# Kernel optimization log

Hardware: AMD Instinct MI355X
Metric: run time of the kernel (lower is better)

Reference implementation:

```python
import jax, jax.numpy as jnp
from jax import lax
import numpy as np

B, T, H, L = 4096, 7, 512, 256
D = 2 * H  # bidirectional LSTM feature dim


def _lstm(x, wih, whh, bih, bhh, reverse):
    # x: [B, T, L]; torch gate order i, f, g, o
    b, hdim = x.shape[0], whh.shape[0]
    xs = jnp.swapaxes(x, 0, 1)  # [T, B, L]
    bias = bih + bhh

    def step(carry, xt):
        h, c = carry
        gates = xt @ wih + h @ whh + bias
        i, f, g, o = jnp.split(gates, 4, axis=-1)
        c = jax.nn.sigmoid(f) * c + jax.nn.sigmoid(i) * jnp.tanh(g)
        h = jax.nn.sigmoid(o) * jnp.tanh(c)
        return (h, c), h

    h0 = jnp.zeros((b, hdim), x.dtype)
    _, hs = lax.scan(step, (h0, h0), xs, reverse=reverse)
    return jnp.swapaxes(hs, 0, 1)  # [B, T, H]


def _att(enc, dec):
    # Sequential attention: keys/values start as enc and grow with each decoder output.
    keys = enc  # [B, T, D]
    outs = []
    for i in range(dec.shape[1]):  # fixed small T=7, Python loop is static
        q = dec[:, i, :]                                  # [B, D]
        scores = jnp.einsum('bd,btd->bt', q, keys)        # dot over features
        a = jax.nn.softmax(scores, axis=1)
        ctx = jnp.einsum('bt,btd->bd', a, keys)
        out = ctx + q
        outs.append(out)
        keys = jnp.concatenate([keys, out[:, None, :]], axis=1)
    return jnp.stack(outs, axis=1)  # [B, T, D]


def _deconv(x, w, b):
    # torch ConvTranspose2d (stride 1, pad 0) == full conv with flipped, in/out-swapped kernel
    kh, kw = w.shape[2], w.shape[3]
    w2 = jnp.transpose(w[:, :, ::-1, ::-1], (1, 0, 2, 3))  # [out, in, kh, kw]
    y = lax.conv_general_dilated(x, w2, (1, 1), ((kh - 1, kh - 1), (kw - 1, kw - 1)),
                                 dimension_numbers=('NCHW', 'OIHW', 'NCHW'))
    return y + b[None, :, None, None]


def setup_inputs() -> dict:
    key = jax.random.key(0)
    ks = jax.random.split(key, 12)
    p = lambda k, shape: jax.random.normal(k, shape, jnp.float32) * 0.02
    return {
        'lstm_enc': jax.random.normal(ks[0], (B, T, D), jnp.float32),
        'gaussian_noise': jax.random.normal(ks[1], (B, L), jnp.float32),
        'embedrep_w': p(ks[2], (L, L * T)), 'embedrep_b': jnp.zeros((L * T,), jnp.float32),
        'wih_f': p(ks[3], (L, 4 * H)), 'whh_f': p(ks[4], (H, 4 * H)),
        'bih_f': jnp.zeros((4 * H,), jnp.float32), 'bhh_f': jnp.zeros((4 * H,), jnp.float32),
        'wih_b': p(ks[5], (L, 4 * H)), 'whh_b': p(ks[6], (H, 4 * H)),
        'bih_b': jnp.zeros((4 * H,), jnp.float32), 'bhh_b': jnp.zeros((4 * H,), jnp.float32),
        'emb_w': p(ks[7], (D, 1024)), 'emb_b': jnp.zeros((1024,), jnp.float32),
        'dc3_w': p(ks[8], (64, 32, 1, 3)), 'dc3_b': jnp.zeros((32,), jnp.float32),
        'dc1_w': p(ks[9], (32, 16, 1, 5)), 'dc1_b': jnp.zeros((16,), jnp.float32),
        'dc2_w': p(ks[10], (16, 1, 3, 3)), 'dc2_b': jnp.zeros((1,), jnp.float32),
        'infer': 0,
    }


def reference(lstm_enc, gaussian_noise, embedrep_w, embedrep_b,
              wih_f, whh_f, bih_f, bhh_f, wih_b, whh_b, bih_b, bhh_b,
              emb_w, emb_b, dc3_w, dc3_b, dc1_w, dc1_b, dc2_w, dc2_b, infer):
    b = lstm_enc.shape[0]
    g1 = jax.nn.soft_sign(gaussian_noise @ embedrep_w + embedrep_b)   # [B, L*T]
    rep = g1.reshape(b, T, L)                                          # [B, 7, L]
    hf = _lstm(rep, wih_f, whh_f, bih_f, bhh_f, False)
    hb = _lstm(rep, wih_b, whh_b, bih_b, bhh_b, True)
    lstm1 = jnp.concatenate([hf, hb], axis=-1)                         # [B, 7, 2H]
    att_out = _att(lstm_enc, lstm1)                                    # [B, 7, 2H]
    emb = att_out @ emb_w + emb_b                                      # [B, 7, 1024]
    up = jax.nn.soft_sign(emb).reshape(b * T, 64, 1, 16)
    x = jax.nn.leaky_relu(_deconv(up, dc3_w, dc3_b))                   # [B*7, 32, 1, 18]
    x = jax.nn.leaky_relu(_deconv(x, dc1_w, dc1_b))                    # [B*7, 16, 1, 22]
    x = jax.nn.leaky_relu(_deconv(x, dc2_w, dc2_b))                    # [B*7, 1, 3, 24]
    x = jax.nn.softmax(x, axis=2)                                      # softmax over H dim (=3)
    out = x.reshape(b, T, 1, 3, 24)[:, :, -1, :, :]                    # [B, 7, 3, 24]
    return out
```

## Files before the change

### kernel.cpp

```cpp
#include <hip/hip_runtime.h>
#include <stdint.h>


typedef __attribute__((ext_vector_type(4))) float f32x4;
typedef __attribute__((ext_vector_type(8))) short bf16x8;
typedef __attribute__((ext_vector_type(4))) unsigned short us4;

__device__ __forceinline__ unsigned short f2b(float f) {
  union { float f; unsigned u; } x; x.f = f;
  unsigned r = x.u + 0x7FFFu + ((x.u >> 16) & 1u);
  return (unsigned short)(r >> 16);
}
__device__ __forceinline__ float b2f(unsigned short s) {
  union { unsigned u; float f; } x; x.u = ((unsigned)s) << 16; return x.f;
}
__device__ __forceinline__ float sigmoidf(float x) {
  return 1.f / (1.f + __expf(-x));
}
__device__ __forceinline__ float fast_tanh(float x) {
  x = fminf(15.f, fmaxf(-15.f, x));
  float e = __expf(2.f * x);
  return (e - 1.f) / (e + 1.f);
}

__device__ __forceinline__ void gl_lds16(const void* g, void* l) {
  auto gp = reinterpret_cast<const __attribute__((address_space(1))) unsigned int*>(
      reinterpret_cast<uintptr_t>(g));
  auto lp = reinterpret_cast<__attribute__((address_space(3))) unsigned int*>(
      reinterpret_cast<uintptr_t>(l));
  __builtin_amdgcn_global_load_lds(gp, lp, 16, 0, 0);
}

__device__ __forceinline__ void stage256x64_swz(const unsigned short* src, int ld,
                                                unsigned short* lds, int tid) {
  const int wv = tid >> 6;
  const int g = (tid & 7) ^ ((tid >> 3) & 7);
  const int rowin = tid >> 3;
#pragma unroll
  for (int r = 0; r < 4; ++r) {
    int row = r * 64 + rowin;
    gl_lds16(src + (size_t)row * ld + g * 8, lds + r * 4096 + wv * 512);
  }
}

__device__ __forceinline__ bf16x8 lds_frag(const unsigned short* base, int row, int ko) {
  return *(const bf16x8*)(base + row * 64 + (ko ^ ((row & 7) << 3)));
}

__device__ __forceinline__ void ktile_256(const unsigned short* As, const unsigned short* Bs,
                                          int wm, int wn, int lane, f32x4 acc[8][4]) {
  const int lr = lane & 15, lq = (lane >> 4) * 8;
  bf16x8 b[4][2];
#pragma unroll
  for (int ni = 0; ni < 4; ++ni) {
    int brow = wn * 64 + ni * 16 + lr;
    b[ni][0] = lds_frag(Bs, brow, lq);
    b[ni][1] = lds_frag(Bs, brow, 32 + lq);
  }
#pragma unroll
  for (int mi = 0; mi < 8; ++mi) {
    int arow = wm * 128 + mi * 16 + lr;
    bf16x8 a0 = lds_frag(As, arow, lq);
    bf16x8 a1 = lds_frag(As, arow, 32 + lq);
#pragma unroll
    for (int ni = 0; ni < 4; ++ni) {
      acc[mi][ni] = __builtin_amdgcn_mfma_f32_16x16x32_bf16(a0, b[ni][0], acc[mi][ni], 0, 0, 0);
      acc[mi][ni] = __builtin_amdgcn_mfma_f32_16x16x32_bf16(a1, b[ni][1], acc[mi][ni], 0, 0, 0);
    }
  }
}

#define KLOOP_GATE(kt, NT)                                         \
  if ((kt) + 1 < (NT)) asm volatile("s_waitcnt vmcnt(8)" ::: "memory"); \
  else                 asm volatile("s_waitcnt vmcnt(0)" ::: "memory"); \
  __builtin_amdgcn_s_barrier();                                    \
  __builtin_amdgcn_sched_barrier(0);

#define KLOOP_FREE()                                               \
  __builtin_amdgcn_sched_barrier(0);                               \
  __builtin_amdgcn_s_barrier();

__device__ __forceinline__ void stage128x64(const unsigned short* src, int ld,
                                            unsigned short* lds, int wv, int lane) {
#pragma unroll
  for (int r = 0; r < 4; ++r) {
    int row = r * 32 + wv * 8 + (lane >> 3);
    gl_lds16(src + (size_t)row * ld + (lane & 7) * 8, lds + (r * 32 + wv * 8) * 64);
  }
}
__device__ __forceinline__ void mfma_tile(const unsigned short* As, const unsigned short* Bs,
                                          int wm, int wn, int lane, f32x4 acc[4][4]) {
#pragma unroll
  for (int kk = 0; kk < 2; ++kk) {
    int ko = kk * 32 + (lane >> 4) * 8;
    bf16x8 a[4], b[4];
#pragma unroll
    for (int i = 0; i < 4; ++i)
      a[i] = *(const bf16x8*)(As + (size_t)(wm * 64 + i * 16 + (lane & 15)) * 64 + ko);
#pragma unroll
    for (int i = 0; i < 4; ++i)
      b[i] = *(const bf16x8*)(Bs + (size_t)(wn * 64 + i * 16 + (lane & 15)) * 64 + ko);
#pragma unroll
    for (int mi = 0; mi < 4; ++mi)
#pragma unroll
      for (int ni = 0; ni < 4; ++ni)
        acc[mi][ni] = __builtin_amdgcn_mfma_f32_16x16x32_bf16(a[mi], b[ni], acc[mi][ni], 0, 0, 0);
  }
}

__global__ __launch_bounds__(256) void pack_kernel(
    const float* __restrict__ noise, const float* __restrict__ erep_w,
    const float* __restrict__ emb_w,
    const float* __restrict__ wih_f, const float* __restrict__ whh_f,
    const float* __restrict__ bih_f, const float* __restrict__ bhh_f,
    const float* __restrict__ wih_b, const float* __restrict__ whh_b,
    const float* __restrict__ bih_b, const float* __restrict__ bhh_b,
    unsigned short* __restrict__ noiseb, unsigned short* __restrict__ erepT,
    unsigned short* __restrict__ embT, unsigned short* __restrict__ lstmW,
    float* __restrict__ lstmB) {
  const int N0 = 4096 * 256;
  const int N1 = 1792 * 256;
  const int N2 = 1024 * 1024;
  const int N3 = 2 * 2048 * 768;
  const int N4 = 2 * 2048;
  const int total = N0 + N1 + N2 + N3 + N4;
  for (int i = blockIdx.x * 256 + threadIdx.x; i < total; i += gridDim.x * 256) {
    int x = i;
    if (x < N0) { noiseb[x] = f2b(noise[x]); continue; }
    x -= N0;
    if (x < N1) { int n = x >> 8, k = x & 255; erepT[x] = f2b(erep_w[k * 1792 + n]); continue; }
    x -= N1;
    if (x < N2) {
      int n = x >> 10, k = x & 1023;
      int o = (n & 63) * 16 + (n >> 6);
      embT[x] = f2b(emb_w[k * 1024 + o]);
      continue;
    }
    x -= N2;
    if (x < N3) {
      int dir = x / (2048 * 768);
      int r = x - dir * (2048 * 768);
      int npk = r / 768, k = r - (r / 768) * 768;
      int blk = npk >> 6, g = (npk >> 4) & 3, u = npk & 15;
      int o = g * 512 + blk * 16 + u;
      const float* wih = dir ? wih_b : wih_f;
      const float* whh = dir ? whh_b : whh_f;
      float v = (k < 256) ? wih[k * 2048 + o] : whh[(k - 256) * 2048 + o];
      lstmW[x] = f2b(v);
      continue;
    }
    x -= N3;
    {
      int dir = x >> 11, npk = x & 2047;
      int blk = npk >> 6, g = (npk >> 4) & 3, u = npk & 15;
      int o = g * 512 + blk * 16 + u;
      lstmB[x] = dir ? (bih_b[o] + bhh_b[o]) : (bih_f[o] + bhh_f[o]);
    }
  }
}

__global__ __launch_bounds__(256) void gemm_rep_kernel(
    const unsigned short* __restrict__ A, const unsigned short* __restrict__ Bt,
    const float* __restrict__ bias, unsigned short* __restrict__ rep_t) {
  __shared__ unsigned short As[128 * 64];
  __shared__ unsigned short Bs[128 * 64];
  const int lane = threadIdx.x & 63, wv = threadIdx.x >> 6;
  const int wm = wv >> 1, wn = wv & 1;
  const int m0 = blockIdx.y * 128, n0 = blockIdx.x * 128;
  f32x4 acc[4][4];
#pragma unroll
  for (int i = 0; i < 4; ++i)
#pragma unroll
    for (int j = 0; j < 4; ++j) acc[i][j] = (f32x4){0.f, 0.f, 0.f, 0.f};
  for (int k0 = 0; k0 < 256; k0 += 64) {
    stage128x64(A + (size_t)m0 * 256 + k0, 256, As, wv, lane);
    stage128x64(Bt + (size_t)n0 * 256 + k0, 256, Bs, wv, lane);
    __syncthreads();
    mfma_tile(As, Bs, wm, wn, lane, acc);
    __syncthreads();
  }
#pragma unroll
  for (int ni = 0; ni < 4; ++ni) {
    int n = n0 + wn * 64 + ni * 16 + (lane & 15);
    float bv = bias[n];
    int t = n >> 8, l = n & 255;
#pragma unroll
    for (int mi = 0; mi < 4; ++mi)
#pragma unroll
      for (int r = 0; r < 4; ++r) {
        int m = m0 + wm * 64 + mi * 16 + (lane >> 4) * 4 + r;
        float v = acc[mi][ni][r] + bv;
        v = v / (1.f + fabsf(v));
        rep_t[((size_t)t * 4096 + m) * 256 + l] = f2b(v);
      }
  }
}

__global__ __launch_bounds__(512, 2) void lstm_step256_kernel(
    const unsigned short* __restrict__ rep_t, const unsigned short* __restrict__ Wp,
    const float* __restrict__ biasP, unsigned short* __restrict__ hbuf,
    float* __restrict__ cbuf, unsigned short* __restrict__ lstm1, int step) {
  __shared__ unsigned short AsB[2][256 * 64];
  __shared__ unsigned short BsB[2][256 * 64];
  const int tid = threadIdx.x, lane = tid & 63, wv = tid >> 6;
  const int wm = wv >> 2, wn = wv & 3;
  const int swz = (blockIdx.x & 7) * 32 + (blockIdx.x >> 3);
  const int dir = swz >> 7;
  const int by = (swz & 127) >> 3, bx = swz & 7;
  const int m0 = by * 256, n0 = bx * 256;
  const int t_proc = dir ? (6 - step) : step;
  const unsigned short* W = Wp + (size_t)dir * 2048 * 768;
  const unsigned short* hin = hbuf + ((size_t)(step & 1) * 2 + dir) * (4096 * 512);
  unsigned short* hout = hbuf + ((size_t)((step + 1) & 1) * 2 + dir) * (4096 * 512);
  float* cp = cbuf + (size_t)dir * (4096 * 512);
  const unsigned short* xsrc = rep_t + (size_t)t_proc * 4096 * 256;

  f32x4 acc[8][4];
#pragma unroll
  for (int i = 0; i < 8; ++i)
#pragma unroll
    for (int j = 0; j < 4; ++j) acc[i][j] = (f32x4){0.f, 0.f, 0.f, 0.f};

#define LSTM_STAGE_A(kt, buf)                                                     \
  if ((kt) < 4) stage256x64_swz(xsrc + (size_t)m0 * 256 + (kt) * 64, 256, AsB[buf], tid); \
  else          stage256x64_swz(hin + (size_t)m0 * 512 + ((kt) - 4) * 64, 512, AsB[buf], tid);

  LSTM_STAGE_A(0, 0)
  stage256x64_swz(W + (size_t)n0 * 768 + 0, 768, BsB[0], tid);
  LSTM_STAGE_A(1, 1)
  stage256x64_swz(W + (size_t)n0 * 768 + 64, 768, BsB[1], tid);

  for (int kt = 0; kt < 12; ++kt) {
    const int cur = kt & 1;
    KLOOP_GATE(kt, 12)
    ktile_256(AsB[cur], BsB[cur], wm, wn, lane, acc);
    KLOOP_FREE()
    if (kt + 2 < 12) {
      LSTM_STAGE_A(kt + 2, cur)
      stage256x64_swz(W + (size_t)n0 * 768 + (kt + 2) * 64, 768, BsB[cur], tid);
    }
  }
#undef LSTM_STAGE_A

  const int u = lane & 15;
  const int blk = (n0 + wn * 64) >> 6;
  const int j = blk * 16 + u;
  const float bz0 = biasP[dir * 2048 + blk * 64 + 0 * 16 + u];
  const float bz1 = biasP[dir * 2048 + blk * 64 + 1 * 16 + u];
  const float bz2 = biasP[dir * 2048 + blk * 64 + 2 * 16 + u];
  const float bz3 = biasP[dir * 2048 + blk * 64 + 3 * 16 + u];
#pragma unroll
  for (int mi = 0; mi < 8; ++mi)
#pragma unroll
    for (int r = 0; r < 4; ++r) {
      int row = m0 + wm * 128 + mi * 16 + (lane >> 4) * 4 + r;
      float gi = acc[mi][0][r] + bz0;
      float gf = acc[mi][1][r] + bz1;
      float gg = acc[mi][2][r] + bz2;
      float go = acc[mi][3][r] + bz3;
      size_t ci = (size_t)row * 512 + j;
      float c = sigmoidf(gf) * cp[ci] + sigmoidf(gi) * fast_tanh(gg);
      cp[ci] = c;
      float h = sigmoidf(go) * fast_tanh(c);
      unsigned short hb = f2b(h);
      hout[ci] = hb;
      lstm1[((size_t)row * 7 + t_proc) * 1024 + dir * 512 + j] = hb;
    }
}

__global__ __launch_bounds__(256) void att_fused2_kernel(
    const float* __restrict__ enc, const unsigned short* __restrict__ lstm1,
    unsigned short* __restrict__ att) {
  __shared__ unsigned short Qs[7 * 1032];
  __shared__ unsigned short Ehs[7 * 1032];
  __shared__ unsigned short Els[7 * 1032];
  __shared__ float P[4 * 2 * 64 * 4];
  __shared__ float sG[98];
  __shared__ float sC[7][14];
  __shared__ float sA[16];
  const int tid = threadIdx.x, lane = tid & 63, wv = tid >> 6;
  const int b = blockIdx.x;
  const float* Eb = enc + (size_t)b * 7168;
  const unsigned short* Qb = lstm1 + (size_t)b * 7168;

  if (tid < 98) ((float*)sC)[tid] = 0.f;

  const f32x4* Eb4 = (const f32x4*)Eb;
#pragma unroll
  for (int r = 0; r < 7; ++r) {
    f32x4 v = Eb4[r * 256 + tid];
    us4 hi, lo;
#pragma unroll
    for (int e = 0; e < 4; ++e) {
      hi[e] = f2b(v[e]);
      lo[e] = f2b(v[e] - b2f(hi[e]));
    }
    *(us4*)&Ehs[r * 1032 + tid * 4] = hi;
    *(us4*)&Els[r * 1032 + tid * 4] = lo;
  }
  const bf16x8* Qb8 = (const bf16x8*)Qb;
#pragma unroll
  for (int r = 0; r < 4; ++r) {
    int idx = r * 256 + tid;
    if (idx < 896) {
      int row = idx >> 7, col = (idx & 127) * 8;
      *(bf16x8*)&Qs[row * 1032 + col] = Qb8[idx];
    }
  }
  __syncthreads();

  {
    const int rr = lane & 15;
    const int rowc = rr > 6 ? 6 : rr;
    const int kbase = wv * 256 + (lane >> 4) * 8;
    f32x4 g1 = {0.f, 0.f, 0.f, 0.f}, g2 = {0.f, 0.f, 0.f, 0.f};
#pragma unroll
    for (int s = 0; s < 8; ++s) {
      const int k0 = kbase + s * 32;
      bf16x8 aq = *(const bf16x8*)&Qs[rowc * 1032 + k0];
      bf16x8 bh = *(const bf16x8*)&Ehs[rowc * 1032 + k0];
      bf16x8 bl = *(const bf16x8*)&Els[rowc * 1032 + k0];
      g1 = __builtin_amdgcn_mfma_f32_16x16x32_bf16(aq, bh, g1, 0, 0, 0);
      g1 = __builtin_amdgcn_mfma_f32_16x16x32_bf16(aq, bl, g1, 0, 0, 0);
      g2 = __builtin_amdgcn_mfma_f32_16x16x32_bf16(aq, aq, g2, 0, 0, 0);
    }
    *(f32x4*)&P[((wv * 2 + 0) * 64 + lane) * 4] = g1;
    *(f32x4*)&P[((wv * 2 + 1) * 64 + lane) * 4] = g2;
  }
  __syncthreads();

  if (tid < 98) {
    int i = tid / 14, v = tid - i * 14;
    int col = v < 7 ? v : v - 7;
    int tile = v < 7 ? 0 : 1;
    int ln = ((i >> 2) << 4) | col;
    int rg = i & 3;
    float s = 0.f;
#pragma unroll
    for (int w = 0; w < 4; ++w) s += P[((w * 2 + tile) * 64 + ln) * 4 + rg];
    sG[i * 14 + v] = s;
  }
  __syncthreads();

  if (wv == 0) {
    for (int i = 0; i < 7; ++i) {
      const int nt = 7 + i;
      float s = -1e30f;
      if (lane < 7) {
        s = sG[i * 14 + lane];
      } else if (lane < nt) {
        int jj = lane - 7;
        float a2 = 0.f;
#pragma unroll
        for (int v = 0; v < 14; ++v) a2 += sC[jj][v] * sG[i * 14 + v];
        s = a2;
      }
      float mx = s;
#pragma unroll
      for (int off = 8; off >= 1; off >>= 1) mx = fmaxf(mx, __shfl_xor(mx, off, 16));
      float e = (lane < nt) ? __expf(s - mx) : 0.f;
      float sum = e;
#pragma unroll
      for (int off = 8; off >= 1; off >>= 1) sum += __shfl_xor(sum, off, 16);
      float a = e / sum;
      if (lane < 16) sA[lane] = a;
      if (lane < 14) {
        float c = (lane < 7) ? sA[lane] : 0.f;
        for (int jj = 0; jj < i; ++jj) c += sA[7 + jj] * sC[jj][lane];
        if (lane == 7 + i) c += 1.f;
        sC[i][lane] = c;
      }
    }
  }
  __syncthreads();

  {
    const int d0 = tid * 4;
    float acc[7][4];
#pragma unroll
    for (int i = 0; i < 7; ++i)
#pragma unroll
      for (int e = 0; e < 4; ++e) acc[i][e] = 0.f;
#pragma unroll
    for (int t = 0; t < 7; ++t) {
      us4 h = *(const us4*)&Ehs[t * 1032 + d0];
      us4 l = *(const us4*)&Els[t * 1032 + d0];
      float ev[4];
#pragma unroll
      for (int e = 0; e < 4; ++e) ev[e] = b2f(h[e]) + b2f(l[e]);
#pragma unroll
      for (int i = 0; i < 7; ++i) {
        float c = sC[i][t];
#pragma unroll
        for (int e = 0; e < 4; ++e) acc[i][e] += c * ev[e];
      }
    }
#pragma unroll
    for (int m = 0; m < 7; ++m) {
      us4 qv = *(const us4*)&Qs[m * 1032 + d0];
      float qf[4];
#pragma unroll
      for (int e = 0; e < 4; ++e) qf[e] = b2f(qv[e]);
#pragma unroll
      for (int i = m; i < 7; ++i) {
        float c = sC[i][7 + m];
#pragma unroll
        for (int e = 0; e < 4; ++e) acc[i][e] += c * qf[e];
      }
    }
    unsigned short* Ab = att + (size_t)b * 7168;
#pragma unroll
    for (int i = 0; i < 7; ++i) {
      us4 r;
#pragma unroll
      for (int e = 0; e < 4; ++e) r[e] = f2b(acc[i][e]);
      *(us4*)(Ab + i * 1024 + d0) = r;
    }
  }
}

__global__ __launch_bounds__(512, 2) void gemm_emb256_kernel(
    const unsigned short* __restrict__ A, const unsigned short* __restrict__ Bt,
    const float* __restrict__ bias, unsigned short* __restrict__ up_t) {
  __shared__ unsigned short AsB[2][256 * 64];
  __shared__ unsigned short BsB[2][256 * 64];
  const int tid = threadIdx.x, lane = tid & 63, wv = tid >> 6;
  const int wm = wv >> 2, wn = wv & 3;
  const int swz = (blockIdx.x & 7) * 56 + (blockIdx.x >> 3);
  const int by = swz >> 2, bx = swz & 3;
  const int m0 = by * 256, n0 = bx * 256;

  f32x4 acc[8][4];
#pragma unroll
  for (int i = 0; i < 8; ++i)
#pragma unroll
    for (int j = 0; j < 4; ++j) acc[i][j] = (f32x4){0.f, 0.f, 0.f, 0.f};

  stage256x64_swz(A + (size_t)m0 * 1024 + 0, 1024, AsB[0], tid);
  stage256x64_swz(Bt + (size_t)n0 * 1024 + 0, 1024, BsB[0], tid);
  stage256x64_swz(A + (size_t)m0 * 1024 + 64, 1024, AsB[1], tid);
  stage256x64_swz(Bt + (size_t)n0 * 1024 + 64, 1024, BsB[1], tid);

  for (int kt = 0; kt < 16; ++kt) {
    const int cur = kt & 1;
    KLOOP_GATE(kt, 16)
    ktile_256(AsB[cur], BsB[cur], wm, wn, lane, acc);
    KLOOP_FREE()
    if (kt + 2 < 16) {
      stage256x64_swz(A + (size_t)m0 * 1024 + (kt + 2) * 64, 1024, AsB[cur], tid);
      stage256x64_swz(Bt + (size_t)n0 * 1024 + (kt + 2) * 64, 1024, BsB[cur], tid);
    }
  }

#pragma unroll
  for (int ni = 0; ni < 4; ++ni) {
    int np = n0 + wn * 64 + ni * 16 + (lane & 15);
    int o = (np & 63) * 16 + (np >> 6);
    float bv = bias[o];
#pragma unroll
    for (int mi = 0; mi < 8; ++mi)
#pragma unroll
      for (int r = 0; r < 4; ++r) {
        int m = m0 + wm * 128 + mi * 16 + (lane >> 4) * 4 + r;
        float v = acc[mi][ni][r] + bv;
        v = v / (1.f + fabsf(v));
        up_t[(size_t)m * 1024 + np] = f2b(v);
      }
  }
}

__global__ __launch_bounds__(256) void dc3_kernel(const unsigned short* __restrict__ up_t,
                                                  const float* __restrict__ w3,
                                                  const float* __restrict__ b3,
                                                  unsigned short* __restrict__ y1_t) {
  const int lane = threadIdx.x & 63, wv = threadIdx.x >> 6;
  const int kq = (lane >> 4) * 8;
  const int oc = lane & 15;
  bf16x8 bf[2][6];
#pragma unroll
  for (int nt = 0; nt < 2; ++nt)
#pragma unroll
    for (int kk = 0; kk < 6; ++kk) {
      bf16x8 v;
#pragma unroll
      for (int t = 0; t < 8; ++t) {
        int k = kk * 32 + kq + t;
        int jj = k >> 6, ic = k & 63;
        v[t] = (short)f2b(w3[((size_t)ic * 32 + nt * 16 + oc) * 3 + jj]);
      }
      bf[nt][kk] = v;
    }
  const float bia0 = b3[oc], bia1 = b3[16 + oc];
  const int base_chunk = blockIdx.x * 32 + wv * 8;
  for (int cc = 0; cc < 8; ++cc) {
    const int chunk = base_chunk + cc;
    int m = chunk * 16 + (lane & 15);
    int img = m / 18, ow = m - img * 18;
    const unsigned short* arow = up_t + (size_t)img * 1024;
    f32x4 acc0 = {0.f, 0.f, 0.f, 0.f}, acc1 = {0.f, 0.f, 0.f, 0.f};
#pragma unroll
    for (int kk = 0; kk < 6; ++kk) {
      int jj = kk >> 1;
      int ic0 = (kk & 1) * 32 + kq;
      int iw = ow - jj;
      bf16x8 a = {0, 0, 0, 0, 0, 0, 0, 0};
      if ((unsigned)iw < 16u) a = *(const bf16x8*)(arow + iw * 64 + ic0);
      acc0 = __builtin_amdgcn_mfma_f32_16x16x32_bf16(a, bf[0][kk], acc0, 0, 0, 0);
      acc1 = __builtin_amdgcn_mfma_f32_16x16x32_bf16(a, bf[1][kk], acc1, 0, 0, 0);
    }
#pragma unroll
    for (int r = 0; r < 4; ++r) {
      int mm = chunk * 16 + (lane >> 4) * 4 + r;
      float v0 = acc0[r] + bia0; v0 = v0 > 0.f ? v0 : 0.01f * v0;
      float v1 = acc1[r] + bia1; v1 = v1 > 0.f ? v1 : 0.01f * v1;
      y1_t[(size_t)mm * 32 + oc] = f2b(v0);
      y1_t[(size_t)mm * 32 + 16 + oc] = f2b(v1);
    }
  }
}

__global__ __launch_bounds__(256) void dc1_kernel(const unsigned short* __restrict__ y1_t,
                                                  const float* __restrict__ w1,
                                                  const float* __restrict__ b1,
                                                  unsigned short* __restrict__ y2_t) {
  const int lane = threadIdx.x & 63, wv = threadIdx.x >> 6;
  const int kq = (lane >> 4) * 8;
  const int oc = lane & 15;
  bf16x8 bf[5];
#pragma unroll
  for (int kk = 0; kk < 5; ++kk) {
    bf16x8 v;
#pragma unroll
    for (int t = 0; t < 8; ++t) {
      int ic = kq + t;
      v[t] = (short)f2b(w1[((size_t)ic * 16 + oc) * 5 + kk]);
    }
    bf[kk] = v;
  }
  const float bia = b1[oc];
  const int base_chunk = blockIdx.x * 32 + wv * 8;
  for (int cc = 0; cc < 8; ++cc) {
    const int chunk = base_chunk + cc;
    int m = chunk * 16 + (lane & 15);
    int img = m / 22, ow = m - img * 22;
    const unsigned short* abase = y1_t + (size_t)img * 18 * 32;
    f32x4 acc = {0.f, 0.f, 0.f, 0.f};
#pragma unroll
    for (int kk = 0; kk < 5; ++kk) {
      int iw = ow - kk;
      bf16x8 a = {0, 0, 0, 0, 0, 0, 0, 0};
      if ((unsigned)iw < 18u) a = *(const bf16x8*)(abase + iw * 32 + kq);
      acc = __builtin_amdgcn_mfma_f32_16x16x32_bf16(a, bf[kk], acc, 0, 0, 0);
    }
#pragma unroll
    for (int r = 0; r < 4; ++r) {
      int mm = chunk * 16 + (lane >> 4) * 4 + r;
      float v = acc[r] + bia;
      v = v > 0.f ? v : 0.01f * v;
      y2_t[(size_t)mm * 16 + oc] = f2b(v);
    }
  }
}

__global__ __launch_bounds__(256) void dc2_kernel(const unsigned short* __restrict__ y2_t,
                                                  const float* __restrict__ w2,
                                                  const float* __restrict__ b2,
                                                  float* __restrict__ out) {
  int idx = blockIdx.x * 256 + threadIdx.x;
  int img = idx / 24, ow = idx - img * 24;
  float lg0 = b2[0], lg1 = b2[0], lg2 = b2[0];
#pragma unroll
  for (int jj = 0; jj < 3; ++jj) {
    int iw = ow - jj;
    if ((unsigned)iw >= 22u) continue;
    const unsigned short* row = y2_t + ((size_t)img * 22 + iw) * 16;
    bf16x8 v0 = *(const bf16x8*)(row);
    bf16x8 v1 = *(const bf16x8*)(row + 8);
    float x[16];
#pragma unroll
    for (int ic = 0; ic < 8; ++ic) {
      x[ic] = b2f((unsigned short)v0[ic]);
      x[8 + ic] = b2f((unsigned short)v1[ic]);
    }
#pragma unroll
    for (int ic = 0; ic < 16; ++ic) {
      lg0 += x[ic] * w2[ic * 9 + 0 * 3 + jj];
      lg1 += x[ic] * w2[ic * 9 + 1 * 3 + jj];
      lg2 += x[ic] * w2[ic * 9 + 2 * 3 + jj];
    }
  }
  lg0 = lg0 > 0.f ? lg0 : 0.01f * lg0;
  lg1 = lg1 > 0.f ? lg1 : 0.01f * lg1;
  lg2 = lg2 > 0.f ? lg2 : 0.01f * lg2;
  float mx = fmaxf(lg0, fmaxf(lg1, lg2));
  float e0 = __expf(lg0 - mx), e1 = __expf(lg1 - mx), e2 = __expf(lg2 - mx);
  float inv = 1.f / (e0 + e1 + e2);
  size_t ob = (size_t)img * 72 + ow;
  out[ob] = e0 * inv;
  out[ob + 24] = e1 * inv;
  out[ob + 48] = e2 * inv;
}

extern "C" void kernel_launch(void* const* d_in, const int* in_sizes, int n_in,
                              void* d_out, int out_size, void* d_ws, size_t ws_size,
                              hipStream_t stream) {
  (void)in_sizes; (void)n_in; (void)out_size; (void)ws_size;
  const float* enc    = (const float*)d_in[0];
  const float* noise  = (const float*)d_in[1];
  const float* erep_w = (const float*)d_in[2];
  const float* erep_b = (const float*)d_in[3];
  const float* wih_f  = (const float*)d_in[4];
  const float* whh_f  = (const float*)d_in[5];
  const float* bih_f  = (const float*)d_in[6];
  const float* bhh_f  = (const float*)d_in[7];
  const float* wih_b  = (const float*)d_in[8];
  const float* whh_b  = (const float*)d_in[9];
  const float* bih_b  = (const float*)d_in[10];
  const float* bhh_b  = (const float*)d_in[11];
  const float* emb_w  = (const float*)d_in[12];
  const float* emb_b  = (const float*)d_in[13];
  const float* dc3w   = (const float*)d_in[14];
  const float* dc3b   = (const float*)d_in[15];
  const float* dc1w   = (const float*)d_in[16];
  const float* dc1b   = (const float*)d_in[17];
  const float* dc2w   = (const float*)d_in[18];
  const float* dc2b   = (const float*)d_in[19];
  float* out = (float*)d_out;

  char* p = (char*)d_ws;
  auto carve = [&p](size_t bytes) {
    char* r = p;
    p += (bytes + 255) & ~(size_t)255;
    return r;
  };
  unsigned short* rep_t  = (unsigned short*)carve(7ull * 4096 * 256 * 2);
  unsigned short* lstmW  = (unsigned short*)carve(2ull * 2048 * 768 * 2);
  float*          lstmB  = (float*)carve(2ull * 2048 * 4);
  unsigned short* noiseb = (unsigned short*)carve(4096ull * 256 * 2);
  unsigned short* erepT  = (unsigned short*)carve(1792ull * 256 * 2);
  unsigned short* embT   = (unsigned short*)carve(1024ull * 1024 * 2);
  unsigned short* hbuf   = (unsigned short*)carve(4ull * 4096 * 512 * 2);
  float*          cbuf   = (float*)carve(2ull * 4096 * 512 * 4);
  unsigned short* lstm1  = (unsigned short*)carve(4096ull * 7 * 1024 * 2);
  unsigned short* att    = (unsigned short*)carve(28672ull * 1024 * 2);
  unsigned short* up_t   = (unsigned short*)carve(28672ull * 1024 * 2);
  unsigned short* y1_t   = (unsigned short*)carve(28672ull * 18 * 32 * 2);
  unsigned short* y2_t   = (unsigned short*)carve(28672ull * 22 * 16 * 2);

  hipMemsetAsync(hbuf, 0, 2ull * 4096 * 512 * 2, stream);
  hipMemsetAsync(cbuf, 0, 2ull * 4096 * 512 * 4, stream);

  pack_kernel<<<2048, 256, 0, stream>>>(noise, erep_w, emb_w, wih_f, whh_f, bih_f, bhh_f,
                                        wih_b, whh_b, bih_b, bhh_b,
                                        noiseb, erepT, embT, lstmW, lstmB);
  gemm_rep_kernel<<<dim3(14, 32), 256, 0, stream>>>(noiseb, erepT, erep_b, rep_t);
  for (int s = 0; s < 7; ++s)
    lstm_step256_kernel<<<256, 512, 0, stream>>>(rep_t, lstmW, lstmB, hbuf, cbuf, lstm1, s);
  att_fused2_kernel<<<4096, 256, 0, stream>>>(enc, lstm1, att);
  gemm_emb256_kernel<<<448, 512, 0, stream>>>(att, embT, emb_b, up_t);
  dc3_kernel<<<1008, 256, 0, stream>>>(up_t, dc3w, dc3b, y1_t);
  dc1_kernel<<<1232, 256, 0, stream>>>(y1_t, dc1w, dc1b, y2_t);
  dc2_kernel<<<2688, 256, 0, stream>>>(y2_t, dc2w, dc2b, out);
}
```

Before: 533.0 us.

## Split K-tiles into half-tiles with fine-grained 8-phase staged MFMA pipeline

Replaces the double-buffered 256x64 K-tile loop in the LSTM step and embedding GEMM kernels with a pipeline over 32-wide half-tiles. Each half-tile is computed in two MFMA phases, and global-to-LDS loads for later half-tiles are issued between phases, gated by per-phase vmcnt waits and barriers. It also adds setprio around the MFMA bursts and a new LDS swizzle for 32-element rows. The aim is to overlap memory traffic with compute more finely and cut pipeline bubbles, at the cost of more barriers and tighter, more fragile waitcnt accounting.

```diff
diff --git a/kernel.cpp b/kernel.cpp
--- a/kernel.cpp
+++ b/kernel.cpp
@@ -31,54 +31,55 @@
   __builtin_amdgcn_global_load_lds(gp, lp, 16, 0, 0);
 }
 
-__device__ __forceinline__ void stage256x64_swz(const unsigned short* src, int ld,
-                                                unsigned short* lds, int tid) {
-  const int wv = tid >> 6;
-  const int g = (tid & 7) ^ ((tid >> 3) & 7);
-  const int rowin = tid >> 3;
-#pragma unroll
-  for (int r = 0; r < 4; ++r) {
-    int row = r * 64 + rowin;
-    gl_lds16(src + (size_t)row * ld + g * 8, lds + r * 4096 + wv * 512);
-  }
-}
-
-__device__ __forceinline__ bf16x8 lds_frag(const unsigned short* base, int row, int ko) {
-  return *(const bf16x8*)(base + row * 64 + (ko ^ ((row & 7) << 3)));
-}
-
-__device__ __forceinline__ void ktile_256(const unsigned short* As, const unsigned short* Bs,
-                                          int wm, int wn, int lane, f32x4 acc[8][4]) {
+
+__device__ __forceinline__ void stage_half(const unsigned short* src, int ld,
+                                           unsigned short* hbase, int tid) {
+  const int row_in = tid >> 2;
+  const int gidx = tid & 3;
+#pragma unroll
+  for (int r = 0; r < 2; ++r) {
+    int row = r * 128 + row_in;
+    int gsrc = gidx ^ ((row >> 1) & 3);
+    gl_lds16(src + (size_t)row * ld + gsrc * 8, hbase + r * 4096 + (tid >> 6) * 512);
+  }
+}
+
+__device__ __forceinline__ bf16x8 lds_fragH(const unsigned short* hbase, int row, int lq) {
+  return *(const bf16x8*)(hbase + row * 32 + (lq ^ (((row >> 1) & 3) << 3)));
+}
+
+__device__ __forceinline__ void gate8() { asm volatile("s_waitcnt vmcnt(8)" ::: "memory"); }
+__device__ __forceinline__ void gate4() { asm volatile("s_waitcnt vmcnt(4)" ::: "memory"); }
+__device__ __forceinline__ void gate0() { asm volatile("s_waitcnt vmcnt(0)" ::: "memory"); }
+
+#define PH_TOP()                         \
+  __builtin_amdgcn_s_barrier();          \
+  __builtin_amdgcn_sched_barrier(0)
+
+template<int MH, bool READB>
+__device__ __forceinline__ void phase_mfma(const unsigned short* Ah, const unsigned short* Bh,
+                                           int wm, int wn, int lane,
+                                           bf16x8 (&bfr)[4], f32x4 (&acc)[8][4]) {
   const int lr = lane & 15, lq = (lane >> 4) * 8;
-  bf16x8 b[4][2];
-#pragma unroll
-  for (int ni = 0; ni < 4; ++ni) {
-    int brow = wn * 64 + ni * 16 + lr;
-    b[ni][0] = lds_frag(Bs, brow, lq);
-    b[ni][1] = lds_frag(Bs, brow, 32 + lq);
-  }
-#pragma unroll
-  for (int mi = 0; mi < 8; ++mi) {
-    int arow = wm * 128 + mi * 16 + lr;
-    bf16x8 a0 = lds_frag(As, arow, lq);
-    bf16x8 a1 = lds_frag(As, arow, 32 + lq);
-#pragma unroll
-    for (int ni = 0; ni < 4; ++ni) {
-      acc[mi][ni] = __builtin_amdgcn_mfma_f32_16x16x32_bf16(a0, b[ni][0], acc[mi][ni], 0, 0, 0);
-      acc[mi][ni] = __builtin_amdgcn_mfma_f32_16x16x32_bf16(a1, b[ni][1], acc[mi][ni], 0, 0, 0);
-    }
-  }
-}
-
-#define KLOOP_GATE(kt, NT)                                         \
-  if ((kt) + 1 < (NT)) asm volatile("s_waitcnt vmcnt(8)" ::: "memory"); \
-  else                 asm volatile("s_waitcnt vmcnt(0)" ::: "memory"); \
-  __builtin_amdgcn_s_barrier();                                    \
+  if (READB) {
+#pragma unroll
+    for (int ni = 0; ni < 4; ++ni) bfr[ni] = lds_fragH(Bh, wn * 64 + ni * 16 + lr, lq);
+  }
+  bf16x8 a[4];
+#pragma unroll
+  for (int i = 0; i < 4; ++i)
+    a[i] = lds_fragH(Ah, wm * 128 + (MH * 4 + i) * 16 + lr, lq);
+  asm volatile("s_waitcnt lgkmcnt(0)" ::: "memory");
   __builtin_amdgcn_sched_barrier(0);
-
-#define KLOOP_FREE()                                               \
-  __builtin_amdgcn_sched_barrier(0);                               \
-  __builtin_amdgcn_s_barrier();
+  __builtin_amdgcn_s_setprio(1);
+#pragma unroll
+  for (int i = 0; i < 4; ++i)
+#pragma unroll
+    for (int ni = 0; ni < 4; ++ni)
+      acc[MH * 4 + i][ni] =
+          __builtin_amdgcn_mfma_f32_16x16x32_bf16(a[i], bfr[ni], acc[MH * 4 + i][ni], 0, 0, 0);
+  __builtin_amdgcn_s_setprio(0);
+}
 
 __device__ __forceinline__ void stage128x64(const unsigned short* src, int ld,
                                             unsigned short* lds, int wv, int lane) {
@@ -200,8 +201,8 @@
     const unsigned short* __restrict__ rep_t, const unsigned short* __restrict__ Wp,
     const float* __restrict__ biasP, unsigned short* __restrict__ hbuf,
     float* __restrict__ cbuf, unsigned short* __restrict__ lstm1, int step) {
-  __shared__ unsigned short AsB[2][256 * 64];
-  __shared__ unsigned short BsB[2][256 * 64];
+  __shared__ unsigned short Ax[2][2][8192];
+  __shared__ unsigned short Bx[2][2][8192];
   const int tid = threadIdx.x, lane = tid & 63, wv = tid >> 6;
   const int wm = wv >> 2, wn = wv & 3;
   const int swz = (blockIdx.x & 7) * 32 + (blockIdx.x >> 3);
@@ -221,26 +222,53 @@
 #pragma unroll
     for (int j = 0; j < 4; ++j) acc[i][j] = (f32x4){0.f, 0.f, 0.f, 0.f};
 
-#define LSTM_STAGE_A(kt, buf)                                                     \
-  if ((kt) < 4) stage256x64_swz(xsrc + (size_t)m0 * 256 + (kt) * 64, 256, AsB[buf], tid); \
-  else          stage256x64_swz(hin + (size_t)m0 * 512 + ((kt) - 4) * 64, 512, AsB[buf], tid);
-
-  LSTM_STAGE_A(0, 0)
-  stage256x64_swz(W + (size_t)n0 * 768 + 0, 768, BsB[0], tid);
-  LSTM_STAGE_A(1, 1)
-  stage256x64_swz(W + (size_t)n0 * 768 + 64, 768, BsB[1], tid);
-
-  for (int kt = 0; kt < 12; ++kt) {
-    const int cur = kt & 1;
-    KLOOP_GATE(kt, 12)
-    ktile_256(AsB[cur], BsB[cur], wm, wn, lane, acc);
-    KLOOP_FREE()
-    if (kt + 2 < 12) {
-      LSTM_STAGE_A(kt + 2, cur)
-      stage256x64_swz(W + (size_t)n0 * 768 + (kt + 2) * 64, 768, BsB[cur], tid);
-    }
-  }
-#undef LSTM_STAGE_A
+#define ASRC_L(kt, h) ((kt) < 4 ? xsrc + (size_t)m0 * 256 + (kt) * 64 + (h) * 32 \
+                                : hin + (size_t)m0 * 512 + ((kt) - 4) * 64 + (h) * 32)
+#define ALD_L(kt) ((kt) < 4 ? 256 : 512)
+#define BSRC_L(kt, h) (W + (size_t)n0 * 768 + (kt) * 64 + (h) * 32)
+
+  stage_half(ASRC_L(0, 0), ALD_L(0), Ax[0][0], tid);
+  stage_half(BSRC_L(0, 0), 768, Bx[0][0], tid);
+  stage_half(ASRC_L(0, 1), ALD_L(0), Ax[0][1], tid);
+  stage_half(BSRC_L(0, 1), 768, Bx[0][1], tid);
+  stage_half(ASRC_L(1, 0), ALD_L(1), Ax[1][0], tid);
+  stage_half(BSRC_L(1, 0), 768, Bx[1][0], tid);
+
+  const int NITER = 6;
+  for (int it = 0; it < NITER; ++it) {
+    const bool last = (it == NITER - 1);
+    const int t1 = 2 * it + 1, t2 = 2 * it + 2, t3 = 2 * it + 3;
+    bf16x8 bfr[4];
+    gate8(); PH_TOP();
+    stage_half(ASRC_L(t1, 1), ALD_L(t1), Ax[1][1], tid);
+    phase_mfma<0, true>(Ax[0][0], Bx[0][0], wm, wn, lane, bfr, acc);
+    PH_TOP();
+    stage_half(BSRC_L(t1, 1), 768, Bx[1][1], tid);
+    phase_mfma<1, false>(Ax[0][0], Bx[0][0], wm, wn, lane, bfr, acc);
+    gate8(); PH_TOP();
+    if (!last) stage_half(ASRC_L(t2, 0), ALD_L(t2), Ax[0][0], tid);
+    phase_mfma<0, true>(Ax[0][1], Bx[0][1], wm, wn, lane, bfr, acc);
+    PH_TOP();
+    if (!last) stage_half(BSRC_L(t2, 0), 768, Bx[0][0], tid);
+    phase_mfma<1, false>(Ax[0][1], Bx[0][1], wm, wn, lane, bfr, acc);
+    if (last) gate4(); else gate8();
+    PH_TOP();
+    if (!last) stage_half(ASRC_L(t2, 1), ALD_L(t2), Ax[0][1], tid);
+    phase_mfma<0, true>(Ax[1][0], Bx[1][0], wm, wn, lane, bfr, acc);
+    PH_TOP();
+    if (!last) stage_half(BSRC_L(t2, 1), 768, Bx[0][1], tid);
+    phase_mfma<1, false>(Ax[1][0], Bx[1][0], wm, wn, lane, bfr, acc);
+    if (last) gate0(); else gate8();
+    PH_TOP();
+    if (!last) stage_half(ASRC_L(t3, 0), ALD_L(t3), Ax[1][0], tid);
+    phase_mfma<0, true>(Ax[1][1], Bx[1][1], wm, wn, lane, bfr, acc);
+    PH_TOP();
+    if (!last) stage_half(BSRC_L(t3, 0), 768, Bx[1][0], tid);
+    phase_mfma<1, false>(Ax[1][1], Bx[1][1], wm, wn, lane, bfr, acc);
+  }
+#undef ASRC_L
+#undef ALD_L
+#undef BSRC_L
 
   const int u = lane & 15;
   const int blk = (n0 + wn * 64) >> 6;
@@ -422,8 +450,8 @@
 __global__ __launch_bounds__(512, 2) void gemm_emb256_kernel(
     const unsigned short* __restrict__ A, const unsigned short* __restrict__ Bt,
     const float* __restrict__ bias, unsigned short* __restrict__ up_t) {
-  __shared__ unsigned short AsB[2][256 * 64];
-  __shared__ unsigned short BsB[2][256 * 64];
+  __shared__ unsigned short Ax[2][2][8192];
+  __shared__ unsigned short Bx[2][2][8192];
   const int tid = threadIdx.x, lane = tid & 63, wv = tid >> 6;
   const int wm = wv >> 2, wn = wv & 3;
   const int swz = (blockIdx.x & 7) * 56 + (blockIdx.x >> 3);
@@ -436,21 +464,50 @@
 #pragma unroll
     for (int j = 0; j < 4; ++j) acc[i][j] = (f32x4){0.f, 0.f, 0.f, 0.f};
 
-  stage256x64_swz(A + (size_t)m0 * 1024 + 0, 1024, AsB[0], tid);
-  stage256x64_swz(Bt + (size_t)n0 * 1024 + 0, 1024, BsB[0], tid);
-  stage256x64_swz(A + (size_t)m0 * 1024 + 64, 1024, AsB[1], tid);
-  stage256x64_swz(Bt + (size_t)n0 * 1024 + 64, 1024, BsB[1], tid);
-
-  for (int kt = 0; kt < 16; ++kt) {
-    const int cur = kt & 1;
-    KLOOP_GATE(kt, 16)
-    ktile_256(AsB[cur], BsB[cur], wm, wn, lane, acc);
-    KLOOP_FREE()
-    if (kt + 2 < 16) {
-      stage256x64_swz(A + (size_t)m0 * 1024 + (kt + 2) * 64, 1024, AsB[cur], tid);
-      stage256x64_swz(Bt + (size_t)n0 * 1024 + (kt + 2) * 64, 1024, BsB[cur], tid);
-    }
-  }
+#define ASRC_E(kt, h) (A + (size_t)m0 * 1024 + (kt) * 64 + (h) * 32)
+#define BSRC_E(kt, h) (Bt + (size_t)n0 * 1024 + (kt) * 64 + (h) * 32)
+
+  stage_half(ASRC_E(0, 0), 1024, Ax[0][0], tid);
+  stage_half(BSRC_E(0, 0), 1024, Bx[0][0], tid);
+  stage_half(ASRC_E(0, 1), 1024, Ax[0][1], tid);
+  stage_half(BSRC_E(0, 1), 1024, Bx[0][1], tid);
+  stage_half(ASRC_E(1, 0), 1024, Ax[1][0], tid);
+  stage_half(BSRC_E(1, 0), 1024, Bx[1][0], tid);
+
+  const int NITER = 8;
+  for (int it = 0; it < NITER; ++it) {
+    const bool last = (it == NITER - 1);
+    const int t1 = 2 * it + 1, t2 = 2 * it + 2, t3 = 2 * it + 3;
+    bf16x8 bfr[4];
+    gate8(); PH_TOP();
+    stage_half(ASRC_E(t1, 1), 1024, Ax[1][1], tid);
+    phase_mfma<0, true>(Ax[0][0], Bx[0][0], wm, wn, lane, bfr, acc);
+    PH_TOP();
+    stage_half(BSRC_E(t1, 1), 1024, Bx[1][1], tid);
+    phase_mfma<1, false>(Ax[0][0], Bx[0][0], wm, wn, lane, bfr, acc);
+    gate8(); PH_TOP();
+    if (!last) stage_half(ASRC_E(t2, 0), 1024, Ax[0][0], tid);
+    phase_mfma<0, true>(Ax[0][1], Bx[0][1], wm, wn, lane, bfr, acc);
+    PH_TOP();
+    if (!last) stage_half(BSRC_E(t2, 0), 1024, Bx[0][0], tid);
+    phase_mfma<1, false>(Ax[0][1], Bx[0][1], wm, wn, lane, bfr, acc);
+    if (last) gate4(); else gate8();
+    PH_TOP();
+    if (!last) stage_half(ASRC_E(t2, 1), 1024, Ax[0][1], tid);
+    phase_mfma<0, true>(Ax[1][0], Bx[1][0], wm, wn, lane, bfr, acc);
+    PH_TOP();
+    if (!last) stage_half(BSRC_E(t2, 1), 1024, Bx[0][1], tid);
+    phase_mfma<1, false>(Ax[1][0], Bx[1][0], wm, wn, lane, bfr, acc);
+    if (last) gate0(); else gate8();
+    PH_TOP();
+    if (!last) stage_half(ASRC_E(t3, 0), 1024, Ax[1][0], tid);
+    phase_mfma<0, true>(Ax[1][1], Bx[1][1], wm, wn, lane, bfr, acc);
+    PH_TOP();
+    if (!last) stage_half(BSRC_E(t3, 0), 1024, Bx[1][0], tid);
+    phase_mfma<1, false>(Ax[1][1], Bx[1][1], wm, wn, lane, bfr, acc);
+  }
+#undef ASRC_E
+#undef BSRC_E
 
 #pragma unroll
   for (int ni = 0; ni < 4; ++ni) {
```

New measurement: 512.4 us. -3.9%, faster.

## Pipeline LSTM and embedding GEMMs with 4-stage K=32 ring buffer

Applied to the files above, without the earlier changes.

Replaces the 2-stage double buffer of 64-wide K tiles with a 4-slot ring of 32-wide K tiles, keeping three tiles of loads in flight. Global-to-LDS staging is interleaved inside the MFMA sequence, with split LDS fragment reads, lgkmcnt waits and s_setprio raised around MFMA bursts. The aim is to hide global load latency and LDS read latency behind matrix math in both the per-step LSTM GEMM and the embedding GEMM. It doubles the number of barriers per K, and the hand-counted vmcnt/lgkmcnt waits and the new swizzle must be exactly right for correctness.

```diff
diff --git a/kernel.cpp b/kernel.cpp
--- a/kernel.cpp
+++ b/kernel.cpp
@@ -31,54 +31,69 @@
   __builtin_amdgcn_global_load_lds(gp, lp, 16, 0, 0);
 }
 
-__device__ __forceinline__ void stage256x64_swz(const unsigned short* src, int ld,
-                                                unsigned short* lds, int tid) {
-  const int wv = tid >> 6;
-  const int g = (tid & 7) ^ ((tid >> 3) & 7);
-  const int rowin = tid >> 3;
-#pragma unroll
-  for (int r = 0; r < 4; ++r) {
-    int row = r * 64 + rowin;
-    gl_lds16(src + (size_t)row * ld + g * 8, lds + r * 4096 + wv * 512);
-  }
-}
-
-__device__ __forceinline__ bf16x8 lds_frag(const unsigned short* base, int row, int ko) {
-  return *(const bf16x8*)(base + row * 64 + (ko ^ ((row & 7) << 3)));
-}
-
-__device__ __forceinline__ void ktile_256(const unsigned short* As, const unsigned short* Bs,
-                                          int wm, int wn, int lane, f32x4 acc[8][4]) {
+
+__device__ __forceinline__ void stage_half(const unsigned short* src, int ld,
+                                           unsigned short* hbase, int tid) {
+  const int row_in = tid >> 2;
+  const int gidx = tid & 3;
+#pragma unroll
+  for (int r = 0; r < 2; ++r) {
+    int row = r * 128 + row_in;
+    int gsrc = gidx ^ ((row >> 1) & 3);
+    gl_lds16(src + (size_t)row * ld + gsrc * 8, hbase + r * 4096 + (tid >> 6) * 512);
+  }
+}
+
+__device__ __forceinline__ bf16x8 lds_fragH(const unsigned short* hbase, int row, int lq) {
+  return *(const bf16x8*)(hbase + row * 32 + (lq ^ (((row >> 1) & 3) << 3)));
+}
+
+template <int N>
+__device__ __forceinline__ void gate() {
+  if constexpr (N == 8) asm volatile("s_waitcnt vmcnt(8)" ::: "memory");
+  else if constexpr (N == 4) asm volatile("s_waitcnt vmcnt(4)" ::: "memory");
+  else asm volatile("s_waitcnt vmcnt(0)" ::: "memory");
+}
+
+#define TILE_TOP(N)                     \
+  gate<N>();                            \
+  __builtin_amdgcn_s_barrier();         \
+  __builtin_amdgcn_sched_barrier(0)
+
+template <class FA, class FB>
+__device__ __forceinline__ void tile32(const unsigned short* Ab, const unsigned short* Bb,
+                                       int wm, int wn, int lane, f32x4 (&acc)[8][4],
+                                       FA stageA, FB stageB) {
   const int lr = lane & 15, lq = (lane >> 4) * 8;
-  bf16x8 b[4][2];
-#pragma unroll
-  for (int ni = 0; ni < 4; ++ni) {
-    int brow = wn * 64 + ni * 16 + lr;
-    b[ni][0] = lds_frag(Bs, brow, lq);
-    b[ni][1] = lds_frag(Bs, brow, 32 + lq);
-  }
-#pragma unroll
-  for (int mi = 0; mi < 8; ++mi) {
-    int arow = wm * 128 + mi * 16 + lr;
-    bf16x8 a0 = lds_frag(As, arow, lq);
-    bf16x8 a1 = lds_frag(As, arow, 32 + lq);
-#pragma unroll
-    for (int ni = 0; ni < 4; ++ni) {
-      acc[mi][ni] = __builtin_amdgcn_mfma_f32_16x16x32_bf16(a0, b[ni][0], acc[mi][ni], 0, 0, 0);
-      acc[mi][ni] = __builtin_amdgcn_mfma_f32_16x16x32_bf16(a1, b[ni][1], acc[mi][ni], 0, 0, 0);
-    }
-  }
-}
-
-#define KLOOP_GATE(kt, NT)                                         \
-  if ((kt) + 1 < (NT)) asm volatile("s_waitcnt vmcnt(8)" ::: "memory"); \
-  else                 asm volatile("s_waitcnt vmcnt(0)" ::: "memory"); \
-  __builtin_amdgcn_s_barrier();                                    \
+  bf16x8 a[8], b[4];
+#pragma unroll
+  for (int i = 0; i < 4; ++i) a[i] = lds_fragH(Ab, wm * 128 + i * 16 + lr, lq);
+#pragma unroll
+  for (int n = 0; n < 4; ++n) b[n] = lds_fragH(Bb, wn * 64 + n * 16 + lr, lq);
   __builtin_amdgcn_sched_barrier(0);
-
-#define KLOOP_FREE()                                               \
-  __builtin_amdgcn_sched_barrier(0);                               \
-  __builtin_amdgcn_s_barrier();
+#pragma unroll
+  for (int i = 4; i < 8; ++i) a[i] = lds_fragH(Ab, wm * 128 + i * 16 + lr, lq);
+  stageA();
+  asm volatile("s_waitcnt lgkmcnt(4)" ::: "memory");
+  __builtin_amdgcn_sched_barrier(0);
+  __builtin_amdgcn_s_setprio(1);
+#pragma unroll
+  for (int i = 0; i < 4; ++i)
+#pragma unroll
+    for (int n = 0; n < 4; ++n)
+      acc[i][n] = __builtin_amdgcn_mfma_f32_16x16x32_bf16(a[i], b[n], acc[i][n], 0, 0, 0);
+  __builtin_amdgcn_s_setprio(0);
+  stageB();
+  asm volatile("s_waitcnt lgkmcnt(0)" ::: "memory");
+  __builtin_amdgcn_sched_barrier(0);
+  __builtin_amdgcn_s_setprio(1);
+#pragma unroll
+  for (int i = 4; i < 8; ++i)
+#pragma unroll
+    for (int n = 0; n < 4; ++n)
+      acc[i][n] = __builtin_amdgcn_mfma_f32_16x16x32_bf16(a[i], b[n], acc[i][n], 0, 0, 0);
+  __builtin_amdgcn_s_setprio(0);
+}
 
 __device__ __forceinline__ void stage128x64(const unsigned short* src, int ld,
                                             unsigned short* lds, int wv, int lane) {
@@ -200,8 +215,8 @@
     const unsigned short* __restrict__ rep_t, const unsigned short* __restrict__ Wp,
     const float* __restrict__ biasP, unsigned short* __restrict__ hbuf,
     float* __restrict__ cbuf, unsigned short* __restrict__ lstm1, int step) {
-  __shared__ unsigned short AsB[2][256 * 64];
-  __shared__ unsigned short BsB[2][256 * 64];
+  __shared__ unsigned short Ar[4][8192];
+  __shared__ unsigned short Br[4][8192];
   const int tid = threadIdx.x, lane = tid & 63, wv = tid >> 6;
   const int wm = wv >> 2, wn = wv & 3;
   const int swz = (blockIdx.x & 7) * 32 + (blockIdx.x >> 3);
@@ -221,26 +236,32 @@
 #pragma unroll
     for (int j = 0; j < 4; ++j) acc[i][j] = (f32x4){0.f, 0.f, 0.f, 0.f};
 
-#define LSTM_STAGE_A(kt, buf)                                                     \
-  if ((kt) < 4) stage256x64_swz(xsrc + (size_t)m0 * 256 + (kt) * 64, 256, AsB[buf], tid); \
-  else          stage256x64_swz(hin + (size_t)m0 * 512 + ((kt) - 4) * 64, 512, AsB[buf], tid);
-
-  LSTM_STAGE_A(0, 0)
-  stage256x64_swz(W + (size_t)n0 * 768 + 0, 768, BsB[0], tid);
-  LSTM_STAGE_A(1, 1)
-  stage256x64_swz(W + (size_t)n0 * 768 + 64, 768, BsB[1], tid);
-
-  for (int kt = 0; kt < 12; ++kt) {
-    const int cur = kt & 1;
-    KLOOP_GATE(kt, 12)
-    ktile_256(AsB[cur], BsB[cur], wm, wn, lane, acc);
-    KLOOP_FREE()
-    if (kt + 2 < 12) {
-      LSTM_STAGE_A(kt + 2, cur)
-      stage256x64_swz(W + (size_t)n0 * 768 + (kt + 2) * 64, 768, BsB[cur], tid);
-    }
-  }
-#undef LSTM_STAGE_A
+  auto asrc = [&](int tt) {
+    return tt < 8 ? xsrc + (size_t)m0 * 256 + tt * 32
+                  : hin + (size_t)m0 * 512 + (tt - 8) * 32;
+  };
+  auto ald = [&](int tt) { return tt < 8 ? 256 : 512; };
+
+  stage_half(asrc(0), ald(0), Ar[0], tid);
+  stage_half(W + (size_t)n0 * 768 + 0 * 32, 768, Br[0], tid);
+  stage_half(asrc(1), ald(1), Ar[1], tid);
+  stage_half(W + (size_t)n0 * 768 + 1 * 32, 768, Br[1], tid);
+  stage_half(asrc(2), ald(2), Ar[2], tid);
+  stage_half(W + (size_t)n0 * 768 + 2 * 32, 768, Br[2], tid);
+
+  for (int t = 0; t <= 20; ++t) {
+    TILE_TOP(8);
+    const int tt = t + 3;
+    tile32(Ar[t & 3], Br[t & 3], wm, wn, lane, acc,
+           [&] { stage_half(asrc(tt), ald(tt), Ar[tt & 3], tid); },
+           [&] { stage_half(W + (size_t)n0 * 768 + tt * 32, 768, Br[tt & 3], tid); });
+  }
+  TILE_TOP(8);
+  tile32(Ar[21 & 3], Br[21 & 3], wm, wn, lane, acc, [&] {}, [&] {});
+  TILE_TOP(4);
+  tile32(Ar[22 & 3], Br[22 & 3], wm, wn, lane, acc, [&] {}, [&] {});
+  TILE_TOP(0);
+  tile32(Ar[23 & 3], Br[23 & 3], wm, wn, lane, acc, [&] {}, [&] {});
 
   const int u = lane & 15;
   const int blk = (n0 + wn * 64) >> 6;
@@ -422,8 +443,8 @@
 __global__ __launch_bounds__(512, 2) void gemm_emb256_kernel(
     const unsigned short* __restrict__ A, const unsigned short* __restrict__ Bt,
     const float* __restrict__ bias, unsigned short* __restrict__ up_t) {
-  __shared__ unsigned short AsB[2][256 * 64];
-  __shared__ unsigned short BsB[2][256 * 64];
+  __shared__ unsigned short Ar[4][8192];
+  __shared__ unsigned short Br[4][8192];
   const int tid = threadIdx.x, lane = tid & 63, wv = tid >> 6;
   const int wm = wv >> 2, wn = wv & 3;
   const int swz = (blockIdx.x & 7) * 56 + (blockIdx.x >> 3);
@@ -436,21 +457,29 @@
 #pragma unroll
     for (int j = 0; j < 4; ++j) acc[i][j] = (f32x4){0.f, 0.f, 0.f, 0.f};
 
-  stage256x64_swz(A + (size_t)m0 * 1024 + 0, 1024, AsB[0], tid);
-  stage256x64_swz(Bt + (size_t)n0 * 1024 + 0, 1024, BsB[0], tid);
-  stage256x64_swz(A + (size_t)m0 * 1024 + 64, 1024, AsB[1], tid);
-  stage256x64_swz(Bt + (size_t)n0 * 1024 + 64, 1024, BsB[1], tid);
-
-  for (int kt = 0; kt < 16; ++kt) {
-    const int cur = kt & 1;
-    KLOOP_GATE(kt, 16)
-    ktile_256(AsB[cur], BsB[cur], wm, wn, lane, acc);
-    KLOOP_FREE()
-    if (kt + 2 < 16) {
-      stage256x64_swz(A + (size_t)m0 * 1024 + (kt + 2) * 64, 1024, AsB[cur], tid);
-      stage256x64_swz(Bt + (size_t)n0 * 1024 + (kt + 2) * 64, 1024, BsB[cur], tid);
-    }
-  }
+  const unsigned short* Abase = A + (size_t)m0 * 1024;
+  const unsigned short* Bbase = Bt + (size_t)n0 * 1024;
+
+  stage_half(Abase + 0 * 32, 1024, Ar[0], tid);
+  stage_half(Bbase + 0 * 32, 1024, Br[0], tid);
+  stage_half(Abase + 1 * 32, 1024, Ar[1], tid);
+  stage_half(Bbase + 1 * 32, 1024, Br[1], tid);
+  stage_half(Abase + 2 * 32, 1024, Ar[2], tid);
+  stage_half(Bbase + 2 * 32, 1024, Br[2], tid);
+
+  for (int t = 0; t <= 28; ++t) {
+    TILE_TOP(8);
+    const int tt = t + 3;
+    tile32(Ar[t & 3], Br[t & 3], wm, wn, lane, acc,
+           [&] { stage_half(Abase + tt * 32, 1024, Ar[tt & 3], tid); },
+           [&] { stage_half(Bbase + tt * 32, 1024, Br[tt & 3], tid); });
+  }
+  TILE_TOP(8);
+  tile32(Ar[29 & 3], Br[29 & 3], wm, wn, lane, acc, [&] {}, [&] {});
+  TILE_TOP(4);
+  tile32(Ar[30 & 3], Br[30 & 3], wm, wn, lane, acc, [&] {}, [&] {});
+  TILE_TOP(0);
+  tile32(Ar[31 & 3], Br[31 & 3], wm, wn, lane, acc, [&] {}, [&] {});
 
 #pragma unroll
   for (int ni = 0; ni < 4; ++ni) {
```

Result: faster. 510.0 us (-4.3%).
